# Optimization experiments

Measured on AMD Instinct MI355X. Metric: run time of the kernel, lower is better.

## Reference

```python
import jax, jax.numpy as jnp
import numpy as np

USER_NUM = 100000
ITEM_NUM = 50000
REC_DIM = 64
N_LAYERS = 3
N_EDGES = 2400000
N_NODES = USER_NUM + ITEM_NUM
BATCH = 4096


def setup_inputs() -> dict:
    key = jax.random.key(0)
    ks = jax.random.split(key, 7)
    user_emb = jax.random.normal(ks[0], (USER_NUM, REC_DIM), dtype=jnp.float32) * 0.1
    item_emb = jax.random.normal(ks[1], (ITEM_NUM, REC_DIM), dtype=jnp.float32) * 0.1
    edge_src = jax.random.randint(ks[2], (N_EDGES,), 0, N_NODES, dtype=jnp.int32)
    edge_dst = jax.random.randint(ks[3], (N_EDGES,), 0, N_NODES, dtype=jnp.int32)
    # symmetric-normalized adjacency values (positive)
    edge_val = jax.random.uniform(ks[4], (N_EDGES,), dtype=jnp.float32)
    users = jax.random.randint(ks[5], (BATCH,), 0, USER_NUM, dtype=jnp.int32)
    items = jax.random.randint(ks[6], (BATCH,), 0, ITEM_NUM, dtype=jnp.int32)
    return {"user_emb": user_emb, "item_emb": item_emb, "edge_src": edge_src,
            "edge_dst": edge_dst, "edge_val": edge_val, "users": users, "items": items}


def _spmm(edge_src, edge_dst, edge_val, emb):
    # out[d] = sum_{e: dst(e)=d} val(e) * emb[src(e)]   (sparse adjacency @ emb)
    msgs = edge_val[:, None] * emb[edge_src]  # [E, d]
    return jax.ops.segment_sum(msgs, edge_dst, num_segments=N_NODES)


def _propagate(user_emb, item_emb, edge_src, edge_dst, edge_val):
    e = jnp.concatenate([user_emb, item_emb], axis=0)  # [N, d]
    acc = e  # running sum instead of stack+mean
    for _ in range(N_LAYERS):
        e = _spmm(edge_src, edge_dst, edge_val, e)
        acc = acc + e
    mean = acc / float(N_LAYERS + 1)
    return mean[:USER_NUM], mean[USER_NUM:]


def reference(user_emb, item_emb, edge_src, edge_dst, edge_val, users, items):
    all_users, all_items = _propagate(user_emb, item_emb, edge_src, edge_dst, edge_val)
    users_emb = all_users[users]  # [B, d]
    items_emb = all_items[items]  # [B, d]
    gamma = jnp.sum(users_emb * items_emb, axis=1)
    return jax.nn.sigmoid(gamma)
```

## Files before the change

kernel.cpp:

```cpp
#include <hip/hip_runtime.h>
#include <hip/hip_bf16.h>
#include <hip/hip_fp16.h>

#define USER_NUM 100000
#define ITEM_NUM 50000
#define NNODES   150000
#define DIM      64
#define NEDGES   2400000
#define BATCH    4096

#define SPN      1024
#define NSUP     ((NNODES + SPN - 1) / SPN)
#define NSUPP    160
#define CHUNK    4096
#define NBLK     ((NEDGES + CHUNK - 1) / CHUNK)
#define INIT_B   ((NNODES * DIM / 4 + 255) / 256)
#define SAMP_B   ((2 * BATCH * 16 + 255) / 256)
#define SPMM_B   ((NNODES * 8 + 255) / 256)

__device__ inline float4 h4_to_f4(float2 raw) {
    __half2 a = ((__half2*)&raw)[0];
    __half2 b = ((__half2*)&raw)[1];
    float2 fa = __half22float2(a);
    float2 fb = __half22float2(b);
    return make_float4(fa.x, fa.y, fb.x, fb.y);
}

__device__ inline float2 f4_to_h4(float4 s) {
    __half2 a = __floats2half2_rn(s.x, s.y);
    __half2 b = __floats2half2_rn(s.z, s.w);
    float2 st;
    ((__half2*)&st)[0] = a;
    ((__half2*)&st)[1] = b;
    return st;
}

__global__ __launch_bounds__(256) void mega1_kernel(
        const int* __restrict__ edge_dst,
        int* __restrict__ bucket_cnt,
        int* __restrict__ blockhist,
        const float* __restrict__ user_emb,
        const float* __restrict__ item_emb,
        __half* __restrict__ curh,
        const int* __restrict__ users,
        const int* __restrict__ items,
        float* __restrict__ acc_s) {
    __shared__ int h[NSUP];
    int b = blockIdx.x;
    if (b < NBLK) {
        for (int t = threadIdx.x; t < NSUP; t += blockDim.x) h[t] = 0;
        __syncthreads();
        int lo = b * CHUNK;
        int hi = min(lo + CHUNK, NEDGES);
        for (int j = lo + (int)threadIdx.x; j < hi; j += blockDim.x)
            atomicAdd(&h[edge_dst[j] >> 10], 1);
        __syncthreads();
        for (int t = threadIdx.x; t < NSUP; t += blockDim.x) {
            int c = h[t];
            blockhist[b * NSUPP + t] = c;
            if (c) atomicAdd(&bucket_cnt[t], c);
        }
    } else if (b < NBLK + INIT_B) {
        const long total4 = (long)NNODES * DIM / 4;
        long i = (long)(b - NBLK) * 256 + threadIdx.x;
        if (i >= total4) return;
        const long user4 = (long)USER_NUM * DIM / 4;
        float4 v;
        if (i < user4) v = ((const float4*)user_emb)[i];
        else           v = ((const float4*)item_emb)[i - user4];
        ((float2*)curh)[i] = f4_to_h4(v);
    } else {
        int t = (b - NBLK - INIT_B) * 256 + threadIdx.x;
        int slot = t >> 4;
        if (slot >= 2 * BATCH) return;
        int k = (t & 15) * 4;
        const float* src = (slot < BATCH)
            ? &user_emb[(long)users[slot] * DIM]
            : &item_emb[(long)items[slot - BATCH] * DIM];
        *(float4*)&acc_s[(long)slot * DIM + k] = *(const float4*)&src[k];
    }
}

__global__ __launch_bounds__(1024) void partition_kernel(
        const int* __restrict__ edge_src,
        const int* __restrict__ edge_dst,
        const float* __restrict__ edge_val,
        const int* __restrict__ blockhist,
        const int* __restrict__ bucket_cnt,
        int* __restrict__ fill,
        int2* __restrict__ tmp) {
    __shared__ int cur_[NSUP];
    __shared__ int goff[NSUP];
    __shared__ long scl[256];
    __shared__ unsigned char sbkt[CHUNK];
    __shared__ int2 sout[CHUNK];
    int tid = threadIdx.x;
    int lo = blockIdx.x * CHUNK;
    int hi = min(lo + CHUNK, NEDGES);
    int n = hi - lo;

    int g = 0, c = 0;
    if (tid < NSUP) {
        g = bucket_cnt[tid];
        c = blockhist[blockIdx.x * NSUPP + tid];
    }
    if (tid < 256) scl[tid] = ((long)g << 32) | (unsigned)c;
    __syncthreads();
    for (int off = 1; off < 256; off <<= 1) {
        long t = (tid >= off && tid < 256) ? scl[tid - off] : 0;
        __syncthreads();
        if (tid < 256) scl[tid] += t;
        __syncthreads();
    }
    if (tid < NSUP) {
        long incl = scl[tid];
        int gincl = (int)(incl >> 32);
        int lincl = (int)(incl & 0xffffffffL);
        int gexcl = gincl - g;
        int lexcl = lincl - c;
        cur_[tid] = lexcl;
        goff[tid] = gexcl + (c ? atomicAdd(&fill[tid], c) : 0) - lexcl;
    }
    __syncthreads();
    for (int i = tid; i < n; i += 1024) {
        int d = edge_dst[lo + i];
        int b = d >> 10;
        int pos = atomicAdd(&cur_[b], 1);
        sout[pos] = make_int2(__float_as_int(edge_val[lo + i]),
                              edge_src[lo + i] | ((d & (SPN - 1)) << 18));
        sbkt[pos] = (unsigned char)b;
    }
    __syncthreads();
    for (int i = tid; i < n; i += 1024) {
        int b = sbkt[i];
        tmp[goff[b] + i] = sout[i];
    }
}

__global__ __launch_bounds__(1024) void local_sort_kernel(
        const int* __restrict__ bucket_cnt,
        const int2* __restrict__ tmp,
        int* __restrict__ row_ptr,
        int2* __restrict__ sedge) {
    __shared__ int gsc[256];
    __shared__ int h[SPN];
    __shared__ int sc[SPN];
    __shared__ int cur[SPN];
    __shared__ int sbase, send;
    int b = blockIdx.x;
    int tid = threadIdx.x;
    int g = (tid < NSUP) ? bucket_cnt[tid] : 0;
    if (tid < 256) gsc[tid] = g;
    __syncthreads();
    for (int off = 1; off < 256; off <<= 1) {
        int t = (tid >= off && tid < 256) ? gsc[tid - off] : 0;
        __syncthreads();
        if (tid < 256) gsc[tid] += t;
        __syncthreads();
    }
    if (tid == 0) {
        int incl = gsc[b];
        int cb = bucket_cnt[b];
        sbase = incl - cb;
        send = incl;
        if (b == 0) row_ptr[NNODES] = NEDGES;
    }
    h[tid] = 0;
    __syncthreads();
    int base = sbase, end = send;
    for (int j = base + tid; j < end; j += 1024)
        atomicAdd(&h[(tmp[j].y >> 18) & (SPN - 1)], 1);
    __syncthreads();
    int c = h[tid];
    sc[tid] = c;
    __syncthreads();
    for (int off = 1; off < SPN; off <<= 1) {
        int t = (tid >= off) ? sc[tid - off] : 0;
        __syncthreads();
        sc[tid] += t;
        __syncthreads();
    }
    int excl = sc[tid] - c;
    cur[tid] = base + excl;
    int node = b * SPN + tid;
    if (node < NNODES) row_ptr[node] = base + excl;
    __syncthreads();
    for (int j = base + tid; j < end; j += 1024) {
        int2 e = tmp[j];
        int dl = (e.y >> 18) & (SPN - 1);
        int pos = atomicAdd(&cur[dl], 1);
        sedge[pos] = make_int2(e.y & 0x3FFFF, e.x);
    }
}

__device__ inline void spmm_body(int gblock, const int* __restrict__ row_ptr,
                                 const int2* __restrict__ sedge,
                                 const __half* __restrict__ cur,
                                 __half* __restrict__ next) {
    long t = (long)gblock * 256 + threadIdx.x;
    int row = (int)(t >> 3);
    if (row >= NNODES) return;
    int k = ((int)t & 7) * 8;
    int start = row_ptr[row];
    int end   = row_ptr[row + 1];
    float a0[8], a1[8], a2[8], a3[8];
    #pragma unroll
    for (int q = 0; q < 8; ++q) { a0[q] = 0.f; a1[q] = 0.f; a2[q] = 0.f; a3[q] = 0.f; }
    int j = start;
    for (; j + 4 <= end; j += 4) {
        int2 e0 = sedge[j];
        int2 e1 = sedge[j + 1];
        int2 e2 = sedge[j + 2];
        int2 e3 = sedge[j + 3];
        float4 r0 = *(const float4*)&cur[(long)e0.x * DIM + k];
        float4 r1 = *(const float4*)&cur[(long)e1.x * DIM + k];
        float4 r2 = *(const float4*)&cur[(long)e2.x * DIM + k];
        float4 r3 = *(const float4*)&cur[(long)e3.x * DIM + k];
        float v0 = __int_as_float(e0.y), v1 = __int_as_float(e1.y);
        float v2 = __int_as_float(e2.y), v3 = __int_as_float(e3.y);
        const __half2* h0 = (const __half2*)&r0;
        const __half2* h1 = (const __half2*)&r1;
        const __half2* h2 = (const __half2*)&r2;
        const __half2* h3 = (const __half2*)&r3;
        #pragma unroll
        for (int q = 0; q < 4; ++q) {
            float2 f0 = __half22float2(h0[q]);
            float2 f1 = __half22float2(h1[q]);
            float2 f2 = __half22float2(h2[q]);
            float2 f3 = __half22float2(h3[q]);
            a0[2*q]   += v0 * f0.x;  a0[2*q+1] += v0 * f0.y;
            a1[2*q]   += v1 * f1.x;  a1[2*q+1] += v1 * f1.y;
            a2[2*q]   += v2 * f2.x;  a2[2*q+1] += v2 * f2.y;
            a3[2*q]   += v3 * f3.x;  a3[2*q+1] += v3 * f3.y;
        }
    }
    for (; j < end; ++j) {
        int2 e = sedge[j];
        float v = __int_as_float(e.y);
        float4 r = *(const float4*)&cur[(long)e.x * DIM + k];
        const __half2* h = (const __half2*)&r;
        #pragma unroll
        for (int q = 0; q < 4; ++q) {
            float2 f = __half22float2(h[q]);
            a0[2*q]   += v * f.x;
            a0[2*q+1] += v * f.y;
        }
    }
    float4 st;
    __half2* sh = (__half2*)&st;
    #pragma unroll
    for (int q = 0; q < 4; ++q) {
        float lo = (a0[2*q]   + a1[2*q])   + (a2[2*q]   + a3[2*q]);
        float hi = (a0[2*q+1] + a1[2*q+1]) + (a2[2*q+1] + a3[2*q+1]);
        sh[q] = __floats2half2_rn(lo, hi);
    }
    *(float4*)&next[(long)row * DIM + k] = st;
}

__global__ void spmm_kernel(const int* __restrict__ row_ptr,
                            const int2* __restrict__ sedge,
                            const __half* __restrict__ cur,
                            __half* __restrict__ next) {
    spmm_body(blockIdx.x, row_ptr, sedge, cur, next);
}

__global__ void spmm_sa_kernel(const int* __restrict__ row_ptr,
                               const int2* __restrict__ sedge,
                               const __half* __restrict__ cur,
                               __half* __restrict__ next,
                               const int* __restrict__ users,
                               const int* __restrict__ items,
                               float* __restrict__ acc_s) {
    if (blockIdx.x < SPMM_B) {
        spmm_body(blockIdx.x, row_ptr, sedge, cur, next);
    } else {
        int t = (blockIdx.x - SPMM_B) * 256 + threadIdx.x;
        int slot = t >> 4;
        if (slot >= 2 * BATCH) return;
        int k = (t & 15) * 4;
        int node = (slot < BATCH) ? users[slot] : USER_NUM + items[slot - BATCH];
        float4 x = h4_to_f4(*(const float2*)&cur[(long)node * DIM + k]);
        long o = (long)slot * DIM + k;
        float4 a = *(float4*)&acc_s[o];
        a.x += x.x; a.y += x.y; a.z += x.z; a.w += x.w;
        *(float4*)&acc_s[o] = a;
    }
}

__global__ __launch_bounds__(256) void pair_kernel(
        const int* __restrict__ row_ptr,
        const int2* __restrict__ sedge,
        const __half* __restrict__ tab,
        const int* __restrict__ users,
        const int* __restrict__ items,
        const float* __restrict__ acc_s,
        float* __restrict__ out) {
    int t = blockIdx.x * 256 + threadIdx.x;
    int p = t >> 5;
    if (p >= BATCH) return;
    int sub = t & 31;
    int lane = threadIdx.x & 63;
    bool isU = (sub < 16);
    int k = (sub & 15) * 4;
    int node = isU ? users[p] : USER_NUM + items[p];
    int slot = isU ? p : BATCH + p;

    int start = row_ptr[node];
    int end   = row_ptr[node + 1];
    float4 s0 = make_float4(0.f, 0.f, 0.f, 0.f);
    float4 s1 = s0;
    int j = start;
    for (; j + 2 <= end; j += 2) {
        int2 e0 = sedge[j];
        int2 e1 = sedge[j + 1];
        float4 x0 = h4_to_f4(*(const float2*)&tab[(long)e0.x * DIM + k]);
        float4 x1 = h4_to_f4(*(const float2*)&tab[(long)e1.x * DIM + k]);
        float v0 = __int_as_float(e0.y), v1 = __int_as_float(e1.y);
        s0.x += v0 * x0.x; s0.y += v0 * x0.y; s0.z += v0 * x0.z; s0.w += v0 * x0.w;
        s1.x += v1 * x1.x; s1.y += v1 * x1.y; s1.z += v1 * x1.z; s1.w += v1 * x1.w;
    }
    for (; j < end; ++j) {
        int2 e = sedge[j];
        float v = __int_as_float(e.y);
        float4 x = h4_to_f4(*(const float2*)&tab[(long)e.x * DIM + k]);
        s0.x += v * x.x; s0.y += v * x.y; s0.z += v * x.z; s0.w += v * x.w;
    }
    float4 a = *(const float4*)&acc_s[(long)slot * DIM + k];
    float4 e2v = h4_to_f4(*(const float2*)&tab[(long)node * DIM + k]);
    a.x += e2v.x + s0.x + s1.x;
    a.y += e2v.y + s0.y + s1.y;
    a.z += e2v.z + s0.z + s1.z;
    a.w += e2v.w + s0.w + s1.w;

    int partner = (lane + 16) & 63;
    float bx = __shfl(a.x, partner);
    float by = __shfl(a.y, partner);
    float bz = __shfl(a.z, partner);
    float bw = __shfl(a.w, partner);
    float pd = a.x * bx + a.y * by + a.z * bz + a.w * bw;
    #pragma unroll
    for (int off = 1; off < 16; off <<= 1) pd += __shfl_xor(pd, off);
    if (sub == 0) {
        float gamma = pd * (1.0f / 16.0f);
        out[p] = 1.0f / (1.0f + __expf(-gamma));
    }
}

extern "C" void kernel_launch(void* const* d_in, const int* in_sizes, int n_in,
                              void* d_out, int out_size, void* d_ws, size_t ws_size,
                              hipStream_t stream) {
    const float* user_emb = (const float*)d_in[0];
    const float* item_emb = (const float*)d_in[1];
    const int*   edge_src = (const int*)d_in[2];
    const int*   edge_dst = (const int*)d_in[3];
    const float* edge_val = (const float*)d_in[4];
    const int*   users    = (const int*)d_in[5];
    const int*   items    = (const int*)d_in[6];
    float* out = (float*)d_out;

    const size_t tbl  = (size_t)NNODES * DIM * sizeof(float);
    const size_t htbl = (size_t)NNODES * DIM * sizeof(__half);
    char* w = (char*)d_ws;
    float*  acc_s       = (float*)w;   w += tbl;
    char*   bufA        = w;           w += tbl;
    char*   bufB        = w;           w += tbl;
    int2*   sedge       = (int2*)w;    w += (size_t)NEDGES * 8;
    int*    row_ptr     = (int*)w;     w += ((size_t)NNODES + 16) * 4;
    int*    bucket_cnt  = (int*)w;     w += ((size_t)NSUP + 8) * 4;
    int*    fill        = (int*)w;     w += ((size_t)NSUP + 8) * 4;
    int*    blockhist   = (int*)w;     w += (size_t)NBLK * NSUPP * 4;

    int2*   tmp   = (int2*)bufA;
    __half* tabA  = (__half*)bufB;
    __half* tabB  = (__half*)(bufB + htbl);

    hipMemsetAsync(bucket_cnt, 0, 2 * ((size_t)NSUP + 8) * 4, stream);
    mega1_kernel<<<NBLK + INIT_B + SAMP_B, 256, 0, stream>>>(
        edge_dst, bucket_cnt, blockhist,
        user_emb, item_emb, tabA, users, items, acc_s);
    partition_kernel<<<NBLK, 1024, 0, stream>>>(edge_src, edge_dst, edge_val,
                                                blockhist, bucket_cnt, fill, tmp);
    local_sort_kernel<<<NSUP, 1024, 0, stream>>>(bucket_cnt, tmp, row_ptr, sedge);
    spmm_kernel<<<SPMM_B, 256, 0, stream>>>(row_ptr, sedge, tabA, tabB);
    spmm_sa_kernel<<<SPMM_B + SAMP_B, 256, 0, stream>>>(row_ptr, sedge, tabB, tabA,
                                                        users, items, acc_s);
    pair_kernel<<<(BATCH * 32 + 255) / 256, 256, 0, stream>>>(
        row_ptr, sedge, tabA, users, items, acc_s, out);
}
```

Before: 202.1 us.

## Restrict second SpMM layer to rows reachable from sampled users and items

While the first SpMM layer runs, extra blocks mark every sampled user/item node and all of its in-neighbors into a deduplicated worklist using atomic flags. The second SpMM layer then computes only those worklist rows instead of all 150k nodes, since the final layer in pair_kernel needs only those rows. With 8192 samples and about 16 edges per row, roughly 130k neighbor marks are made, so the worklist may still cover most nodes. The change also adds atomic contention, an indirect row lookup, and a larger memset for the flag array.

```diff
diff --git a/kernel.cpp b/kernel.cpp
--- a/kernel.cpp
+++ b/kernel.cpp
@@ -17,6 +17,7 @@
 #define INIT_B   ((NNODES * DIM / 4 + 255) / 256)
 #define SAMP_B   ((2 * BATCH * 16 + 255) / 256)
 #define SPMM_B   ((NNODES * 8 + 255) / 256)
+#define MARK_B   ((2 * BATCH + 255) / 256)
 
 __device__ inline float4 h4_to_f4(float2 raw) {
     __half2 a = ((__half2*)&raw)[0];
@@ -193,14 +194,11 @@
     }
 }
 
-__device__ inline void spmm_body(int gblock, const int* __restrict__ row_ptr,
-                                 const int2* __restrict__ sedge,
-                                 const __half* __restrict__ cur,
-                                 __half* __restrict__ next) {
-    long t = (long)gblock * 256 + threadIdx.x;
-    int row = (int)(t >> 3);
-    if (row >= NNODES) return;
-    int k = ((int)t & 7) * 8;
+__device__ inline void spmm_row(int row, int k,
+                                const int* __restrict__ row_ptr,
+                                const int2* __restrict__ sedge,
+                                const __half* __restrict__ cur,
+                                __half* __restrict__ next) {
     int start = row_ptr[row];
     int end   = row_ptr[row + 1];
     float a0[8], a1[8], a2[8], a3[8];
@@ -257,22 +255,51 @@
     *(float4*)&next[(long)row * DIM + k] = st;
 }
 
-__global__ void spmm_kernel(const int* __restrict__ row_ptr,
-                            const int2* __restrict__ sedge,
-                            const __half* __restrict__ cur,
-                            __half* __restrict__ next) {
-    spmm_body(blockIdx.x, row_ptr, sedge, cur, next);
-}
-
-__global__ void spmm_sa_kernel(const int* __restrict__ row_ptr,
-                               const int2* __restrict__ sedge,
-                               const __half* __restrict__ cur,
-                               __half* __restrict__ next,
-                               const int* __restrict__ users,
-                               const int* __restrict__ items,
-                               float* __restrict__ acc_s) {
+__global__ void spmm_mark_kernel(const int* __restrict__ row_ptr,
+                                 const int2* __restrict__ sedge,
+                                 const __half* __restrict__ cur,
+                                 __half* __restrict__ next,
+                                 const int* __restrict__ users,
+                                 const int* __restrict__ items,
+                                 int* __restrict__ flags,
+                                 int* __restrict__ wl,
+                                 int* __restrict__ wl_cnt) {
     if (blockIdx.x < SPMM_B) {
-        spmm_body(blockIdx.x, row_ptr, sedge, cur, next);
+        long t = (long)blockIdx.x * 256 + threadIdx.x;
+        int row = (int)(t >> 3);
+        if (row >= NNODES) return;
+        spmm_row(row, ((int)t & 7) * 8, row_ptr, sedge, cur, next);
+    } else {
+        int s = (blockIdx.x - SPMM_B) * 256 + threadIdx.x;
+        if (s >= 2 * BATCH) return;
+        int node = (s < BATCH) ? users[s] : USER_NUM + items[s - BATCH];
+        if (atomicExch(&flags[node], 1) == 0)
+            wl[atomicAdd(wl_cnt, 1)] = node;
+        int start = row_ptr[node];
+        int end   = row_ptr[node + 1];
+        for (int j = start; j < end; ++j) {
+            int src = sedge[j].x;
+            if (atomicExch(&flags[src], 1) == 0)
+                wl[atomicAdd(wl_cnt, 1)] = src;
+        }
+    }
+}
+
+__global__ void spmm_wl_sa_kernel(const int* __restrict__ row_ptr,
+                                  const int2* __restrict__ sedge,
+                                  const __half* __restrict__ cur,
+                                  __half* __restrict__ next,
+                                  const int* __restrict__ users,
+                                  const int* __restrict__ items,
+                                  float* __restrict__ acc_s,
+                                  const int* __restrict__ wl,
+                                  const int* __restrict__ wl_cnt) {
+    if (blockIdx.x < SPMM_B) {
+        long t = (long)blockIdx.x * 256 + threadIdx.x;
+        int slot = (int)(t >> 3);
+        if (slot >= *wl_cnt) return;
+        int row = wl[slot];
+        spmm_row(row, ((int)t & 7) * 8, row_ptr, sedge, cur, next);
     } else {
         int t = (blockIdx.x - SPMM_B) * 256 + threadIdx.x;
         int slot = t >> 4;
@@ -368,22 +395,27 @@
     int*    row_ptr     = (int*)w;     w += ((size_t)NNODES + 16) * 4;
     int*    bucket_cnt  = (int*)w;     w += ((size_t)NSUP + 8) * 4;
     int*    fill        = (int*)w;     w += ((size_t)NSUP + 8) * 4;
+    int*    wl_cnt      = (int*)w;     w += 16;
+    int*    flags       = (int*)w;     w += (size_t)NNODES * 4;
+    const size_t zero_bytes = (size_t)((char*)w - (char*)bucket_cnt);
+    int*    wl          = (int*)w;     w += (size_t)NNODES * 4;
     int*    blockhist   = (int*)w;     w += (size_t)NBLK * NSUPP * 4;
 
     int2*   tmp   = (int2*)bufA;
     __half* tabA  = (__half*)bufB;
     __half* tabB  = (__half*)(bufB + htbl);
 
-    hipMemsetAsync(bucket_cnt, 0, 2 * ((size_t)NSUP + 8) * 4, stream);
+    hipMemsetAsync(bucket_cnt, 0, zero_bytes, stream);
     mega1_kernel<<<NBLK + INIT_B + SAMP_B, 256, 0, stream>>>(
         edge_dst, bucket_cnt, blockhist,
         user_emb, item_emb, tabA, users, items, acc_s);
     partition_kernel<<<NBLK, 1024, 0, stream>>>(edge_src, edge_dst, edge_val,
                                                 blockhist, bucket_cnt, fill, tmp);
     local_sort_kernel<<<NSUP, 1024, 0, stream>>>(bucket_cnt, tmp, row_ptr, sedge);
-    spmm_kernel<<<SPMM_B, 256, 0, stream>>>(row_ptr, sedge, tabA, tabB);
-    spmm_sa_kernel<<<SPMM_B + SAMP_B, 256, 0, stream>>>(row_ptr, sedge, tabB, tabA,
-                                                        users, items, acc_s);
+    spmm_mark_kernel<<<SPMM_B + MARK_B, 256, 0, stream>>>(
+        row_ptr, sedge, tabA, tabB, users, items, flags, wl, wl_cnt);
+    spmm_wl_sa_kernel<<<SPMM_B + SAMP_B, 256, 0, stream>>>(
+        row_ptr, sedge, tabB, tabA, users, items, acc_s, wl, wl_cnt);
     pair_kernel<<<(BATCH * 32 + 255) / 256, 256, 0, stream>>>(
         row_ptr, sedge, tabA, users, items, acc_s, out);
 }
```

After: 224.0 us. 10.8% more time.
